# Optimization experiments

Hardware: AMD Instinct MI355X
Metric: run time of the kernel (lower is better)

Reference implementation:

```python
import jax, jax.numpy as jnp
import numpy as np
from jax.scipy.special import logsumexp


def setup_inputs() -> dict:
    key = jax.random.key(0)
    k = jax.random.split(key, 8)
    B, T, K, L = 32, 128, 16, 16
    s = 0.05
    y_batch = jax.random.uniform(k[0], (B, T, 1, 28, 28), dtype=jnp.float32)
    enc_w1 = jax.random.normal(k[1], (400, 784), dtype=jnp.float32) * s
    enc_b1 = jnp.zeros((400,), jnp.float32)
    enc_w2 = jax.random.normal(k[2], (2 * L, 400), dtype=jnp.float32) * s
    enc_b2 = jnp.zeros((2 * L,), jnp.float32)
    dec_fc_w = jax.random.normal(k[3], (400, L + K), dtype=jnp.float32) * s
    dec_fc_b = jnp.zeros((400,), jnp.float32)
    dec_w = jax.random.normal(k[4], (784, 400), dtype=jnp.float32) * s
    dec_b = jnp.zeros((784,), jnp.float32)
    log_pi = jnp.zeros((K,), jnp.float32)
    log_A = jax.random.normal(k[5], (K, K), dtype=jnp.float32)
    log_A = log_A.at[jnp.arange(K), jnp.arange(K)].set(-1e9)  # fill_diagonal_(-1e9)
    eps = jax.random.normal(k[6], (B * T, L), dtype=jnp.float32)
    return dict(y_batch=y_batch, enc_w1=enc_w1, enc_b1=enc_b1, enc_w2=enc_w2,
                enc_b2=enc_b2, dec_fc_w=dec_fc_w, dec_fc_b=dec_fc_b, dec_w=dec_w,
                dec_b=dec_b, log_pi=log_pi, log_A=log_A, eps=eps)


def reference(y_batch, enc_w1, enc_b1, enc_w2, enc_b2, dec_fc_w, dec_fc_b,
              dec_w, dec_b, log_pi, log_A, eps):
    B, T = y_batch.shape[0], y_batch.shape[1]
    K = log_pi.shape[0]
    L = eps.shape[1]
    N = B * T
    # ---- VAE emission log-likelihoods (compute_log_bk); dropout in eval mode ----
    y_flat = y_batch.reshape(N, 784)
    h = jax.nn.relu(y_flat @ enc_w1.T + enc_b1)                 # [N,400]
    ml = h @ enc_w2.T + enc_b2                                   # [N,2L]
    mu, logvar = ml[:, :L], ml[:, L:]
    z = mu + eps * jnp.exp(0.5 * logvar)                         # reparameterize
    # decode(z, one_hot(k)) for all k at once: split cat-linear into z part + k column
    Wz, Wx = dec_fc_w[:, :L], dec_fc_w[:, L:]                    # [400,L],[400,K]
    base = z @ Wz.T + dec_fc_b                                   # [N,400]
    hk = jax.nn.relu(base[None, :, :] + Wx.T[:, None, :])        # [K,N,400]
    y_rec = jax.nn.sigmoid(jnp.einsum('knh,oh->kno', hk, dec_w) + dec_b)  # [K,N,784]
    # binary_cross_entropy with torch's log clamp at -100
    logp = jnp.clip(jnp.log(y_rec), -100.0, None)
    log1mp = jnp.clip(jnp.log(1.0 - y_rec), -100.0, None)
    bce = -(y_flat[None] * logp + (1.0 - y_flat[None]) * log1mp)  # [K,N,784]
    recon = bce.sum(-1) / 100.0                                   # [K,N]
    log_bk = (-recon).reshape(K, B, T).transpose(1, 2, 0)         # [B,T,K]
    # ---- forward-backward in log domain ----
    lp = jnp.log(jax.nn.softmax(log_pi) + 1e-9)
    lA = jnp.log(jax.nn.softmax(log_A, axis=1) + 1e-9)
    lb_rest = jnp.moveaxis(log_bk[:, 1:], 1, 0)                   # [T-1,B,K]
    a0 = lp + log_bk[:, 0]                                        # [B,K]

    def fstep(prev, lb_t):
        cur = logsumexp(prev[:, :, None] + lA[None], axis=1) + lb_t
        return cur, cur

    _, alphas = jax.lax.scan(fstep, a0, lb_rest)
    log_alpha = jnp.concatenate([a0[:, None], jnp.moveaxis(alphas, 0, 1)], axis=1)  # [B,T,K]

    bT = jnp.zeros((B, K), log_bk.dtype)

    def bstep(nxt, lb_t1):
        cur = logsumexp(lA[None] + (lb_t1 + nxt)[:, None, :], axis=2)
        return cur, cur

    _, betas = jax.lax.scan(bstep, bT, lb_rest, reverse=True)     # betas[t] = beta_t, t=0..T-2
    log_beta = jnp.concatenate([jnp.moveaxis(betas, 0, 1), bT[:, None]], axis=1)  # [B,T,K]

    lg = log_alpha + log_beta
    log_gamma = lg - logsumexp(lg, axis=2, keepdims=True)

    lxi = (log_alpha[:, :-1, :, None] + lA[None, None]
           + (log_bk[:, 1:] + log_beta[:, 1:])[:, :, None, :])    # [B,T-1,K,K]
    lxi = lxi - logsumexp(lxi, axis=(2, 3), keepdims=True)
    return jnp.exp(log_gamma), jnp.exp(lxi)
```

## Files before the change

kernel.cpp:

```cpp
#include <hip/hip_runtime.h>
#include <math.h>


typedef _Float16 h8v __attribute__((ext_vector_type(8)));
typedef _Float16 h4v __attribute__((ext_vector_type(4)));
typedef float f16v __attribute__((ext_vector_type(16)));

__global__ __launch_bounds__(256)
void k_prep(const float* __restrict__ dw, const float* __restrict__ ew1,
            _Float16* __restrict__ dwh, _Float16* __restrict__ w1h) {
  int idx = blockIdx.x * 256 + threadIdx.x;
  if (idx < 896 * 448) {
    int o = idx / 448, h2 = idx - o * 448;
    float v = (o < 784 && h2 < 400) ? dw[o * 400 + h2] : 0.f;
    dwh[idx] = (_Float16)v;
  } else if (idx < 896 * 448 + 512 * 800) {
    int j = idx - 896 * 448;
    int i = j / 800, kc = j - i * 800;
    float v = (i < 400 && kc < 784) ? ew1[i * 784 + kc] : 0.f;
    w1h[j] = (_Float16)v;
  }
}

#define E1ST 40
__global__ __launch_bounds__(256, 2)
void k_enc1(const float* __restrict__ y, const _Float16* __restrict__ w1h,
            const float* __restrict__ b1, float* __restrict__ hout) {
  __shared__ __align__(16) _Float16 Ah[64 * E1ST];
  __shared__ __align__(16) _Float16 Bh[128 * E1ST];
  const int tid = threadIdx.x;
  const int i0 = blockIdx.x * 128;
  const int n0 = blockIdx.y * 64;
  const int wav = tid >> 6, lane = tid & 63;
  const int wn = wav >> 1, wi = wav & 1;
  const int ln = lane & 31, kg = lane >> 5;

  f16v acc[2];
#pragma unroll
  for (int j = 0; j < 2; ++j)
#pragma unroll
    for (int r = 0; r < 16; ++r) acc[j][r] = 0.f;

  const int ar = tid >> 3, ac4 = (tid & 7) * 4;
  const int br = tid >> 2, bg = (tid & 3) * 8;

#pragma unroll 1
  for (int hc = 0; hc < 25; ++hc) {
    const int h0 = hc * 32;
    __syncthreads();
#pragma unroll
    for (int it = 0; it < 2; ++it) {
      int r = ar + 32 * it;
      float4 a = make_float4(0.f, 0.f, 0.f, 0.f);
      if (h0 + ac4 < 784) a = *(const float4*)&y[(n0 + r) * 784 + h0 + ac4];
      h4v hv;
      hv[0] = (_Float16)a.x; hv[1] = (_Float16)a.y;
      hv[2] = (_Float16)a.z; hv[3] = (_Float16)a.w;
      *(h4v*)&Ah[r * E1ST + ac4] = hv;
    }
#pragma unroll
    for (int it = 0; it < 2; ++it) {
      int r = br + 64 * it;
      *(h8v*)&Bh[r * E1ST + bg] = *(const h8v*)&w1h[(i0 + r) * 800 + h0 + bg];
    }
    __syncthreads();
#pragma unroll
    for (int kk = 0; kk < 2; ++kk) {
      const int ko = kk * 16 + kg * 8;
      h8v a  = *(const h8v*)&Ah[(wn * 32 + ln) * E1ST + ko];
      h8v b0 = *(const h8v*)&Bh[(wi * 64 + ln) * E1ST + ko];
      h8v b1 = *(const h8v*)&Bh[(wi * 64 + 32 + ln) * E1ST + ko];
      acc[0] = __builtin_amdgcn_mfma_f32_32x32x16_f16(a, b0, acc[0], 0, 0, 0);
      acc[1] = __builtin_amdgcn_mfma_f32_32x32x16_f16(a, b1, acc[1], 0, 0, 0);
    }
  }
#pragma unroll
  for (int j = 0; j < 2; ++j) {
    const int i = i0 + wi * 64 + j * 32 + ln;
    if (i < 400) {
      const float bias = b1[i];
#pragma unroll
      for (int reg = 0; reg < 16; ++reg) {
        const int row = n0 + wn * 32 + (reg & 3) + 8 * (reg >> 2) + 4 * kg;
        hout[row * 400 + i] = fmaxf(acc[j][reg] + bias, 0.f);
      }
    }
  }
}

__global__ __launch_bounds__(128, 4)
void k_enc2z(const float* __restrict__ h, const float* __restrict__ w2,
             const float* __restrict__ b2, const float* __restrict__ eps,
             float* __restrict__ z) {
  __shared__ __align__(16) float h_lds[4 * 400];
  __shared__ __align__(16) float w2_lds[32 * 404];
  __shared__ float ml_lds[4 * 32];
  const int tid = threadIdx.x;
  const int n0 = blockIdx.x * 4;
  for (int idx = tid; idx < 400; idx += 128) {
    int r = idx / 100, c = idx % 100;
    *(float4*)&h_lds[r * 400 + c * 4] = *(const float4*)&h[(n0 + r) * 400 + c * 4];
  }
  for (int idx = tid; idx < 3200; idx += 128) {
    int r = idx / 100, c = idx % 100;
    *(float4*)&w2_lds[r * 404 + c * 4] = *(const float4*)&w2[r * 400 + c * 4];
  }
  __syncthreads();
  const int c_ = tid & 31, n_ = tid >> 5;
  float acc = 0.f;
  for (int q = 0; q < 100; ++q) {
    float4 hv = *(const float4*)&h_lds[n_ * 400 + q * 4];
    float4 wv = *(const float4*)&w2_lds[c_ * 404 + q * 4];
    acc += hv.x * wv.x + hv.y * wv.y + hv.z * wv.z + hv.w * wv.w;
  }
  ml_lds[n_ * 32 + c_] = acc + b2[c_];
  __syncthreads();
  if (tid < 64) {
    int n2 = tid >> 4, l = tid & 15;
    float mu = ml_lds[n2 * 32 + l];
    float lv = ml_lds[n2 * 32 + 16 + l];
    z[(n0 + n2) * 16 + l] = mu + eps[(n0 + n2) * 16 + l] * expf(0.5f * lv);
  }
}

__global__ __launch_bounds__(256, 4)
void k_base(const float* __restrict__ z, const float* __restrict__ dfw,
            const float* __restrict__ dfb, float* __restrict__ basep) {
  __shared__ float z_lds[16 * 16];
  __shared__ __align__(16) float wz_lds[400 * 20];
  const int tid = threadIdx.x;
  const int n0 = blockIdx.x * 16;
  if (tid < 64) {
    int n = tid >> 2, c = (tid & 3) * 4;
    *(float4*)&z_lds[n * 16 + c] = *(const float4*)&z[(n0 + n) * 16 + c];
  }
  for (int idx = tid; idx < 1600; idx += 256) {
    int i = idx >> 2, c = (idx & 3) * 4;
    *(float4*)&wz_lds[i * 20 + c] = *(const float4*)&dfw[i * 32 + c];
  }
  __syncthreads();
  for (int idx = tid; idx < 7168; idx += 256) {
    int n = idx / 448, i = idx - n * 448;
    float acc = 0.f;
    if (i < 400) {
      acc = dfb[i];
#pragma unroll
      for (int q = 0; q < 4; ++q) {
        float4 zv = *(const float4*)&z_lds[n * 16 + q * 4];
        float4 wv = *(const float4*)&wz_lds[i * 20 + q * 4];
        acc += zv.x * wv.x + zv.y * wv.y + zv.z * wv.z + zv.w * wv.w;
      }
    }
    basep[(n0 + n) * 448 + i] = acc;
  }
}

#define DST 72
__global__ __launch_bounds__(256, 2)
void k_dec(const float* __restrict__ basep, const float* __restrict__ dfw,
           const _Float16* __restrict__ dwh, const float* __restrict__ decb,
           const float* __restrict__ y, float* __restrict__ lb) {
  __shared__ __align__(16) _Float16 Ah[128 * DST];
  __shared__ __align__(16) _Float16 Bh[128 * DST];
  __shared__ float wx[448];
  __shared__ float red[256];

  const int tid = threadIdx.x;
  const int k = blockIdx.x;
  const int n0 = blockIdx.y * 128;
  const int wav = tid >> 6, lane = tid & 63;
  const int wn = wav >> 1, wo = wav & 1;
  const int ln = lane & 31, kg = lane >> 5;

  for (int i = tid; i < 448; i += 256) wx[i] = (i < 400) ? dfw[i * 32 + 16 + k] : 0.f;

  float pr[2][16];
#pragma unroll
  for (int i = 0; i < 2; ++i)
#pragma unroll
    for (int r = 0; r < 16; ++r) pr[i][r] = 0.f;

  const int ar = tid >> 4, ac4 = (tid & 15) * 4;
  const int br = tid >> 3, bg = (tid & 7) * 8;
  const float* aptr = basep + (long)(n0 + ar) * 448 + ac4;

  float4 apf[8];
#pragma unroll
  for (int it = 0; it < 8; ++it) apf[it] = *(const float4*)&aptr[(16 * it) * 448];

#pragma unroll 1
  for (int ot = 0; ot < 7; ++ot) {
    const int o0 = ot * 128;
    const bool full = (ot < 6);
    f16v acc[2][2];
#pragma unroll
    for (int i = 0; i < 2; ++i)
#pragma unroll
      for (int j = 0; j < 2; ++j)
#pragma unroll
        for (int r = 0; r < 16; ++r) acc[i][j][r] = 0.f;

#pragma unroll 1
    for (int hc = 0; hc < 7; ++hc) {
      const int h0 = hc * 64;
      h8v bpf[4];
#pragma unroll
      for (int it = 0; it < 4; ++it)
        bpf[it] = *(const h8v*)&dwh[(o0 + br + 32 * it) * 448 + h0 + bg];
      __syncthreads();
      {
        float4 w = *(const float4*)&wx[h0 + ac4];
#pragma unroll
        for (int it = 0; it < 8; ++it) {
          int r = ar + 16 * it;
          h4v hv;
          hv[0] = (_Float16)fmaxf(apf[it].x + w.x, 0.f);
          hv[1] = (_Float16)fmaxf(apf[it].y + w.y, 0.f);
          hv[2] = (_Float16)fmaxf(apf[it].z + w.z, 0.f);
          hv[3] = (_Float16)fmaxf(apf[it].w + w.w, 0.f);
          *(h4v*)&Ah[r * DST + ac4] = hv;
        }
      }
#pragma unroll
      for (int it = 0; it < 4; ++it)
        *(h8v*)&Bh[(br + 32 * it) * DST + bg] = bpf[it];
      __syncthreads();
      if (!(ot == 6 && hc == 6)) {
        const int hn = (hc == 6) ? 0 : (hc + 1) * 64;
#pragma unroll
        for (int it = 0; it < 8; ++it)
          apf[it] = *(const float4*)&aptr[(16 * it) * 448 + hn];
      }
#pragma unroll
      for (int kk = 0; kk < 4; ++kk) {
        const int ko = kk * 16 + kg * 8;
        h8v a0 = *(const h8v*)&Ah[(wn * 64 + ln) * DST + ko];
        h8v a1 = *(const h8v*)&Ah[(wn * 64 + 32 + ln) * DST + ko];
        h8v b0 = *(const h8v*)&Bh[(wo * 64 + ln) * DST + ko];
        h8v b1 = *(const h8v*)&Bh[(wo * 64 + 32 + ln) * DST + ko];
        if (full) {
          acc[0][0] = __builtin_amdgcn_mfma_f32_32x32x16_f16(a0, b0, acc[0][0], 0, 0, 0);
          acc[1][0] = __builtin_amdgcn_mfma_f32_32x32x16_f16(a1, b0, acc[1][0], 0, 0, 0);
          acc[0][1] = __builtin_amdgcn_mfma_f32_32x32x16_f16(a0, b1, acc[0][1], 0, 0, 0);
          acc[1][1] = __builtin_amdgcn_mfma_f32_32x32x16_f16(a1, b1, acc[1][1], 0, 0, 0);
        } else if (wo == 0) {
          acc[0][0] = __builtin_amdgcn_mfma_f32_32x32x16_f16(a0, b0, acc[0][0], 0, 0, 0);
          acc[1][0] = __builtin_amdgcn_mfma_f32_32x32x16_f16(a1, b0, acc[1][0], 0, 0, 0);
        }
      }
    }
#pragma unroll
    for (int j = 0; j < 2; ++j) {
      const int o = o0 + wo * 64 + j * 32 + ln;
      const bool valid = (o < 784);
      const float bias = valid ? decb[o] : 0.f;
#pragma unroll
      for (int i = 0; i < 2; ++i) {
        if (valid) {
#pragma unroll
          for (int reg = 0; reg < 16; ++reg) {
            const int row = wn * 64 + i * 32 + (reg & 3) + 8 * (reg >> 2) + 4 * kg;
            float x = acc[i][j][reg] + bias;
            float yv = y[(n0 + row) * 784 + o];
            float spx = fmaxf(x, 0.f) + __logf(1.f + __expf(-fabsf(x)));
            float t2 = fminf(spx, 100.f);
            float t1 = fminf(spx - x, 100.f);
            pr[i][reg] += t2 + yv * (t1 - t2);
          }
        }
      }
    }
  }
#pragma unroll
  for (int i = 0; i < 2; ++i)
#pragma unroll
    for (int reg = 0; reg < 16; ++reg) {
      float v = pr[i][reg];
      v += __shfl_xor(v, 1, 64);
      v += __shfl_xor(v, 2, 64);
      v += __shfl_xor(v, 4, 64);
      v += __shfl_xor(v, 8, 64);
      v += __shfl_xor(v, 16, 64);
      if (ln == 0) {
        const int row = wn * 64 + i * 32 + (reg & 3) + 8 * (reg >> 2) + 4 * kg;
        red[wo * 128 + row] = v;
      }
    }
  __syncthreads();
  if (tid < 128) {
    float s = red[tid] + red[128 + tid];
    lb[(n0 + tid) * 16 + k] = -(s / 100.0f);
  }
}

__global__ __launch_bounds__(256, 2)
void k_hmm(const float* __restrict__ lb, const float* __restrict__ lpi,
           const float* __restrict__ lA, float* __restrict__ out,
           float* __restrict__ g_ah, float* __restrict__ g_pb,
           float* __restrict__ g_sinv, float* __restrict__ g_Al) {
  __shared__ float btl[128 * 16];
  __shared__ float ah[128 * 16];
  __shared__ float bh[128 * 16];
  __shared__ float braw[128 * 16];
  __shared__ float A_l[16 * 17];
  __shared__ float pi_l[16];
  const int tid = threadIdx.x;
  const int b = blockIdx.x;

  for (int idx = tid; idx < 512; idx += 256)
    *(float4*)&btl[idx * 4] = *(const float4*)&lb[b * 2048 + idx * 4];
  if (tid < 16) {
    const int j = tid;
    float m = -1e30f;
#pragma unroll
    for (int q = 0; q < 16; ++q) m = fmaxf(m, lA[j * 16 + q]);
    float e[16]; float s = 0.f;
#pragma unroll
    for (int q = 0; q < 16; ++q) { e[q] = expf(lA[j * 16 + q] - m); s += e[q]; }
    float inv = 1.f / s;
#pragma unroll
    for (int q = 0; q < 16; ++q) {
      float v = e[q] * inv + 1e-9f;
      A_l[j * 17 + q] = v;
      g_Al[j * 16 + q] = v;
    }
  } else if (tid == 16) {
    float m = -1e30f;
#pragma unroll
    for (int q = 0; q < 16; ++q) m = fmaxf(m, lpi[q]);
    float e[16]; float s = 0.f;
#pragma unroll
    for (int q = 0; q < 16; ++q) { e[q] = expf(lpi[q] - m); s += e[q]; }
    float inv = 1.f / s;
#pragma unroll
    for (int q = 0; q < 16; ++q) pi_l[q] = e[q] * inv + 1e-9f;
  }
  __syncthreads();
  if (tid < 128) {
    const int t = tid;
    float v[16]; float m = -1e30f;
#pragma unroll
    for (int q = 0; q < 16; ++q) { v[q] = btl[t * 16 + q]; m = fmaxf(m, v[q]); }
#pragma unroll
    for (int q = 0; q < 16; ++q) btl[t * 16 + q] = expf(v[q] - m);
  }
  __syncthreads();
  const int lane = tid & 63;
  const int kk = lane & 15, grp = lane >> 4;
  if (tid < 64) {
    float v0 = pi_l[kk] * btl[kk];
    float ss0 = v0;
    ss0 += __shfl_xor(ss0, 1, 64); ss0 += __shfl_xor(ss0, 2, 64);
    ss0 += __shfl_xor(ss0, 4, 64); ss0 += __shfl_xor(ss0, 8, 64);
    if (grp == 0) ah[kk] = v0 / ss0;
    for (int t = 1; t < 128; ++t) {
      float acc = 0.f;
#pragma unroll
      for (int jj = 0; jj < 4; ++jj) {
        int j = grp * 4 + jj;
        acc = fmaf(ah[(t - 1) * 16 + j], A_l[j * 17 + kk], acc);
      }
      acc += __shfl_xor(acc, 16, 64);
      acc += __shfl_xor(acc, 32, 64);
      float v = acc * btl[t * 16 + kk];
      float ss = v;
      ss += __shfl_xor(ss, 1, 64); ss += __shfl_xor(ss, 2, 64);
      ss += __shfl_xor(ss, 4, 64); ss += __shfl_xor(ss, 8, 64);
      if (grp == 0) ah[t * 16 + kk] = v / ss;
    }
  } else if (tid < 128) {
    if (grp == 0) bh[127 * 16 + kk] = 1.f;
    for (int t = 126; t >= 0; --t) {
      float acc = 0.f;
#pragma unroll
      for (int q = 0; q < 4; ++q) {
        int k2 = grp * 4 + q;
        acc = fmaf(A_l[kk * 17 + k2], btl[(t + 1) * 16 + k2] * bh[(t + 1) * 16 + k2], acc);
      }
      acc += __shfl_xor(acc, 16, 64);
      acc += __shfl_xor(acc, 32, 64);
      float ss = acc;
      ss += __shfl_xor(ss, 1, 64); ss += __shfl_xor(ss, 2, 64);
      ss += __shfl_xor(ss, 4, 64); ss += __shfl_xor(ss, 8, 64);
      if (grp == 0) { braw[t * 16 + kk] = acc; bh[t * 16 + kk] = acc / ss; }
    }
  }
  __syncthreads();
  if (tid < 128) {
    const int t = tid;
    float g[16]; float s2 = 0.f;
#pragma unroll
    for (int q = 0; q < 16; ++q) { g[q] = ah[t * 16 + q] * bh[t * 16 + q]; s2 += g[q]; }
    float inv = 1.f / s2;
#pragma unroll
    for (int c = 0; c < 4; ++c) {
      float4 o;
      o.x = g[c * 4 + 0] * inv; o.y = g[c * 4 + 1] * inv;
      o.z = g[c * 4 + 2] * inv; o.w = g[c * 4 + 3] * inv;
      *(float4*)&out[(b * 128 + t) * 16 + c * 4] = o;
      float4 av = *(float4*)&ah[t * 16 + c * 4];
      *(float4*)&g_ah[(b * 128 + t) * 16 + c * 4] = av;
      float4 p;
      p.x = btl[t * 16 + c * 4 + 0] * bh[t * 16 + c * 4 + 0];
      p.y = btl[t * 16 + c * 4 + 1] * bh[t * 16 + c * 4 + 1];
      p.z = btl[t * 16 + c * 4 + 2] * bh[t * 16 + c * 4 + 2];
      p.w = btl[t * 16 + c * 4 + 3] * bh[t * 16 + c * 4 + 3];
      *(float4*)&g_pb[(b * 128 + t) * 16 + c * 4] = p;
    }
  } else {
    const int t = tid - 128;
    if (t < 127) {
      float s2 = 0.f;
#pragma unroll
      for (int q = 0; q < 16; ++q) s2 += ah[t * 16 + q] * braw[t * 16 + q];
      g_sinv[b * 128 + t] = 1.f / s2;
    }
  }
}

__global__ __launch_bounds__(256)
void k_xi(const float* __restrict__ g_ah, const float* __restrict__ g_pb,
          const float* __restrict__ g_sinv, const float* __restrict__ g_Al,
          float* __restrict__ out) {
  const int b = blockIdx.x, t = blockIdx.y;
  const int tid = threadIdx.x;
  const int j = tid >> 4, k2 = tid & 15;
  float val = g_ah[(b * 128 + t) * 16 + j] * g_Al[j * 16 + k2] *
              g_pb[(b * 128 + t + 1) * 16 + k2] * g_sinv[b * 128 + t];
  out[65536 + (b * 127 + t) * 256 + tid] = val;
}

extern "C" void kernel_launch(void* const* d_in, const int* in_sizes, int n_in,
                              void* d_out, int out_size, void* d_ws, size_t ws_size,
                              hipStream_t stream) {
  (void)in_sizes; (void)n_in; (void)out_size; (void)ws_size;
  const float* y   = (const float*)d_in[0];
  const float* ew1 = (const float*)d_in[1];
  const float* eb1 = (const float*)d_in[2];
  const float* ew2 = (const float*)d_in[3];
  const float* eb2 = (const float*)d_in[4];
  const float* dfw = (const float*)d_in[5];
  const float* dfb = (const float*)d_in[6];
  const float* dw  = (const float*)d_in[7];
  const float* db  = (const float*)d_in[8];
  const float* lpi = (const float*)d_in[9];
  const float* lA  = (const float*)d_in[10];
  const float* eps = (const float*)d_in[11];
  float* out = (float*)d_out;

  float* ws = (float*)d_ws;
  float* h      = ws;
  float* basep  = ws;
  float* z      = ws + 1835008;
  float* lb     = z + 65536;
  _Float16* dwh = (_Float16*)(lb + 65536);
  _Float16* w1h = dwh + 896 * 448;
  float* g_ah   = (float*)(w1h + 512 * 800);
  float* g_pb   = g_ah + 65536;
  float* g_sinv = g_pb + 65536;
  float* g_Al   = g_sinv + 4096;

  k_prep<<<3168, 256, 0, stream>>>(dw, ew1, dwh, w1h);
  k_enc1<<<dim3(4, 64), 256, 0, stream>>>(y, w1h, eb1, h);
  k_enc2z<<<1024, 128, 0, stream>>>(h, ew2, eb2, eps, z);
  k_base<<<256, 256, 0, stream>>>(z, dfw, dfb, basep);
  k_dec<<<dim3(16, 32), 256, 0, stream>>>(basep, dfw, dwh, db, y, lb);
  k_hmm<<<32, 256, 0, stream>>>(lb, lpi, lA, out, g_ah, g_pb, g_sinv, g_Al);
  k_xi<<<dim3(32, 127), 256, 0, stream>>>(g_ah, g_pb, g_sinv, g_Al, out);
}
```

Before: 338.9 us.

## Fuse encoder stages, split decoder over output tiles, fold xi into HMM kernel

Several changes at once. The w1 fp16 pre-conversion moves into k_enc1, which now converts on the fly and writes h as fp16. enc2, z and base are fused into a single k_ezb kernel that also zeroes lb. k_dec is split so each block handles one output tile, giving 3584 blocks with prefetched B tiles, and partial BCE sums are accumulated into lb with atomicAdd. The HMM forward/backward recursions now keep data in registers and shuffles with rcp instead of division, and the xi output kernel is merged into k_hmm. Together these remove launches and intermediate traffic, at the cost of atomics and a per-block basep reload for every output tile.

```diff
diff --git a/kernel.cpp b/kernel.cpp
--- a/kernel.cpp
+++ b/kernel.cpp
@@ -7,25 +7,19 @@
 typedef float f16v __attribute__((ext_vector_type(16)));
 
 __global__ __launch_bounds__(256)
-void k_prep(const float* __restrict__ dw, const float* __restrict__ ew1,
-            _Float16* __restrict__ dwh, _Float16* __restrict__ w1h) {
+void k_prep(const float* __restrict__ dw, _Float16* __restrict__ dwh) {
   int idx = blockIdx.x * 256 + threadIdx.x;
   if (idx < 896 * 448) {
     int o = idx / 448, h2 = idx - o * 448;
     float v = (o < 784 && h2 < 400) ? dw[o * 400 + h2] : 0.f;
     dwh[idx] = (_Float16)v;
-  } else if (idx < 896 * 448 + 512 * 800) {
-    int j = idx - 896 * 448;
-    int i = j / 800, kc = j - i * 800;
-    float v = (i < 400 && kc < 784) ? ew1[i * 784 + kc] : 0.f;
-    w1h[j] = (_Float16)v;
   }
 }
 
 #define E1ST 40
 __global__ __launch_bounds__(256, 2)
-void k_enc1(const float* __restrict__ y, const _Float16* __restrict__ w1h,
-            const float* __restrict__ b1, float* __restrict__ hout) {
+void k_enc1(const float* __restrict__ y, const float* __restrict__ w1,
+            const float* __restrict__ b1, _Float16* __restrict__ hout) {
   __shared__ __align__(16) _Float16 Ah[64 * E1ST];
   __shared__ __align__(16) _Float16 Bh[128 * E1ST];
   const int tid = threadIdx.x;
@@ -42,7 +36,6 @@
     for (int r = 0; r < 16; ++r) acc[j][r] = 0.f;
 
   const int ar = tid >> 3, ac4 = (tid & 7) * 4;
-  const int br = tid >> 2, bg = (tid & 3) * 8;
 
 #pragma unroll 1
   for (int hc = 0; hc < 25; ++hc) {
@@ -59,9 +52,16 @@
       *(h4v*)&Ah[r * E1ST + ac4] = hv;
     }
 #pragma unroll
-    for (int it = 0; it < 2; ++it) {
-      int r = br + 64 * it;
-      *(h8v*)&Bh[r * E1ST + bg] = *(const h8v*)&w1h[(i0 + r) * 800 + h0 + bg];
+    for (int it = 0; it < 4; ++it) {
+      int idx = tid + it * 256;
+      int r = idx >> 3, c4 = (idx & 7) * 4;
+      int gi = i0 + r, gh = h0 + c4;
+      float4 v = make_float4(0.f, 0.f, 0.f, 0.f);
+      if (gi < 400 && gh + 3 < 784) v = *(const float4*)&w1[gi * 784 + gh];
+      h4v hv;
+      hv[0] = (_Float16)v.x; hv[1] = (_Float16)v.y;
+      hv[2] = (_Float16)v.z; hv[3] = (_Float16)v.w;
+      *(h4v*)&Bh[r * E1ST + c4] = hv;
     }
     __syncthreads();
 #pragma unroll
@@ -69,9 +69,9 @@
       const int ko = kk * 16 + kg * 8;
       h8v a  = *(const h8v*)&Ah[(wn * 32 + ln) * E1ST + ko];
       h8v b0 = *(const h8v*)&Bh[(wi * 64 + ln) * E1ST + ko];
-      h8v b1 = *(const h8v*)&Bh[(wi * 64 + 32 + ln) * E1ST + ko];
+      h8v b1v = *(const h8v*)&Bh[(wi * 64 + 32 + ln) * E1ST + ko];
       acc[0] = __builtin_amdgcn_mfma_f32_32x32x16_f16(a, b0, acc[0], 0, 0, 0);
-      acc[1] = __builtin_amdgcn_mfma_f32_32x32x16_f16(a, b1, acc[1], 0, 0, 0);
+      acc[1] = __builtin_amdgcn_mfma_f32_32x32x16_f16(a, b1v, acc[1], 0, 0, 0);
     }
   }
 #pragma unroll
@@ -82,61 +82,47 @@
 #pragma unroll
       for (int reg = 0; reg < 16; ++reg) {
         const int row = n0 + wn * 32 + (reg & 3) + 8 * (reg >> 2) + 4 * kg;
-        hout[row * 400 + i] = fmaxf(acc[j][reg] + bias, 0.f);
-      }
-    }
-  }
-}
-
-__global__ __launch_bounds__(128, 4)
-void k_enc2z(const float* __restrict__ h, const float* __restrict__ w2,
-             const float* __restrict__ b2, const float* __restrict__ eps,
-             float* __restrict__ z) {
-  __shared__ __align__(16) float h_lds[4 * 400];
-  __shared__ __align__(16) float w2_lds[32 * 404];
-  __shared__ float ml_lds[4 * 32];
-  const int tid = threadIdx.x;
-  const int n0 = blockIdx.x * 4;
-  for (int idx = tid; idx < 400; idx += 128) {
-    int r = idx / 100, c = idx % 100;
-    *(float4*)&h_lds[r * 400 + c * 4] = *(const float4*)&h[(n0 + r) * 400 + c * 4];
-  }
-  for (int idx = tid; idx < 3200; idx += 128) {
-    int r = idx / 100, c = idx % 100;
-    *(float4*)&w2_lds[r * 404 + c * 4] = *(const float4*)&w2[r * 400 + c * 4];
-  }
-  __syncthreads();
-  const int c_ = tid & 31, n_ = tid >> 5;
-  float acc = 0.f;
-  for (int q = 0; q < 100; ++q) {
-    float4 hv = *(const float4*)&h_lds[n_ * 400 + q * 4];
-    float4 wv = *(const float4*)&w2_lds[c_ * 404 + q * 4];
-    acc += hv.x * wv.x + hv.y * wv.y + hv.z * wv.z + hv.w * wv.w;
-  }
-  ml_lds[n_ * 32 + c_] = acc + b2[c_];
-  __syncthreads();
-  if (tid < 64) {
-    int n2 = tid >> 4, l = tid & 15;
-    float mu = ml_lds[n2 * 32 + l];
-    float lv = ml_lds[n2 * 32 + 16 + l];
-    z[(n0 + n2) * 16 + l] = mu + eps[(n0 + n2) * 16 + l] * expf(0.5f * lv);
-  }
-}
-
-__global__ __launch_bounds__(256, 4)
-void k_base(const float* __restrict__ z, const float* __restrict__ dfw,
-            const float* __restrict__ dfb, float* __restrict__ basep) {
-  __shared__ float z_lds[16 * 16];
-  __shared__ __align__(16) float wz_lds[400 * 20];
+        hout[row * 400 + i] = (_Float16)fmaxf(acc[j][reg] + bias, 0.f);
+      }
+    }
+  }
+}
+
+__global__ __launch_bounds__(256, 2)
+void k_ezb(const _Float16* __restrict__ h, const float* __restrict__ w2,
+           const float* __restrict__ b2, const float* __restrict__ eps,
+           const float* __restrict__ dfw, const float* __restrict__ dfb,
+           float* __restrict__ basep, float* __restrict__ lb) {
+  __shared__ __align__(16) float h_lds[16 * 400];
+  __shared__ float ml[16 * 32];
+  __shared__ float zs[16 * 16];
   const int tid = threadIdx.x;
   const int n0 = blockIdx.x * 16;
-  if (tid < 64) {
-    int n = tid >> 2, c = (tid & 3) * 4;
-    *(float4*)&z_lds[n * 16 + c] = *(const float4*)&z[(n0 + n) * 16 + c];
-  }
-  for (int idx = tid; idx < 1600; idx += 256) {
-    int i = idx >> 2, c = (idx & 3) * 4;
-    *(float4*)&wz_lds[i * 20 + c] = *(const float4*)&dfw[i * 32 + c];
+  for (int idx = tid; idx < 800; idx += 256) {
+    int r = idx / 50, c8 = (idx % 50) * 8;
+    h8v v = *(const h8v*)&h[(n0 + r) * 400 + c8];
+#pragma unroll
+    for (int e = 0; e < 8; ++e) h_lds[r * 400 + c8 + e] = (float)v[e];
+  }
+  lb[n0 * 16 + tid] = 0.f;
+  __syncthreads();
+#pragma unroll
+  for (int it = 0; it < 2; ++it) {
+    int task = tid + it * 256;
+    int c = task & 31, n = task >> 5;
+    float acc = 0.f;
+    for (int q = 0; q < 100; ++q) {
+      float4 hv = *(const float4*)&h_lds[n * 400 + q * 4];
+      float4 wv = *(const float4*)&w2[c * 400 + q * 4];
+      acc += hv.x * wv.x + hv.y * wv.y + hv.z * wv.z + hv.w * wv.w;
+    }
+    ml[n * 32 + c] = acc + b2[c];
+  }
+  __syncthreads();
+  {
+    int n = tid >> 4, l = tid & 15;
+    float mu = ml[n * 32 + l], lv = ml[n * 32 + 16 + l];
+    zs[n * 16 + l] = mu + eps[(n0 + n) * 16 + l] * expf(0.5f * lv);
   }
   __syncthreads();
   for (int idx = tid; idx < 7168; idx += 256) {
@@ -146,8 +132,8 @@
       acc = dfb[i];
 #pragma unroll
       for (int q = 0; q < 4; ++q) {
-        float4 zv = *(const float4*)&z_lds[n * 16 + q * 4];
-        float4 wv = *(const float4*)&wz_lds[i * 20 + q * 4];
+        float4 zv = *(const float4*)&zs[n * 16 + q * 4];
+        float4 wv = *(const float4*)&dfw[i * 32 + q * 4];
         acc += zv.x * wv.x + zv.y * wv.y + zv.z * wv.z + zv.w * wv.w;
       }
     }
@@ -166,144 +152,137 @@
   __shared__ float red[256];
 
   const int tid = threadIdx.x;
-  const int k = blockIdx.x;
-  const int n0 = blockIdx.y * 128;
+  const int w = blockIdx.x;
+  const int ot = w >> 9;
+  const int r0 = w & 511;
+  const int k  = (r0 >> 3) & 15;
+  const int nt = (r0 & 7) + 8 * (r0 >> 7);
+  const int n0 = nt * 128;
+  const int o0 = ot * 128;
+  const bool full = (ot < 6);
+
   const int wav = tid >> 6, lane = tid & 63;
   const int wn = wav >> 1, wo = wav & 1;
   const int ln = lane & 31, kg = lane >> 5;
 
   for (int i = tid; i < 448; i += 256) wx[i] = (i < 400) ? dfw[i * 32 + 16 + k] : 0.f;
 
-  float pr[2][16];
-#pragma unroll
-  for (int i = 0; i < 2; ++i)
-#pragma unroll
-    for (int r = 0; r < 16; ++r) pr[i][r] = 0.f;
-
   const int ar = tid >> 4, ac4 = (tid & 15) * 4;
   const int br = tid >> 3, bg = (tid & 7) * 8;
   const float* aptr = basep + (long)(n0 + ar) * 448 + ac4;
 
   float4 apf[8];
+  h8v bpf[4];
 #pragma unroll
   for (int it = 0; it < 8; ++it) apf[it] = *(const float4*)&aptr[(16 * it) * 448];
+#pragma unroll
+  for (int it = 0; it < 4; ++it)
+    bpf[it] = *(const h8v*)&dwh[(o0 + br + 32 * it) * 448 + bg];
+
+  f16v acc[2][2];
+#pragma unroll
+  for (int i = 0; i < 2; ++i)
+#pragma unroll
+    for (int j = 0; j < 2; ++j)
+#pragma unroll
+      for (int r = 0; r < 16; ++r) acc[i][j][r] = 0.f;
 
 #pragma unroll 1
-  for (int ot = 0; ot < 7; ++ot) {
-    const int o0 = ot * 128;
-    const bool full = (ot < 6);
-    f16v acc[2][2];
-#pragma unroll
-    for (int i = 0; i < 2; ++i)
-#pragma unroll
-      for (int j = 0; j < 2; ++j)
-#pragma unroll
-        for (int r = 0; r < 16; ++r) acc[i][j][r] = 0.f;
-
-#pragma unroll 1
-    for (int hc = 0; hc < 7; ++hc) {
-      const int h0 = hc * 64;
-      h8v bpf[4];
+  for (int hc = 0; hc < 7; ++hc) {
+    const int h0 = hc * 64;
+    __syncthreads();
+    {
+      float4 wv = *(const float4*)&wx[h0 + ac4];
+#pragma unroll
+      for (int it = 0; it < 8; ++it) {
+        int rr = ar + 16 * it;
+        h4v hv;
+        hv[0] = (_Float16)fmaxf(apf[it].x + wv.x, 0.f);
+        hv[1] = (_Float16)fmaxf(apf[it].y + wv.y, 0.f);
+        hv[2] = (_Float16)fmaxf(apf[it].z + wv.z, 0.f);
+        hv[3] = (_Float16)fmaxf(apf[it].w + wv.w, 0.f);
+        *(h4v*)&Ah[rr * DST + ac4] = hv;
+      }
+    }
+#pragma unroll
+    for (int it = 0; it < 4; ++it)
+      *(h8v*)&Bh[(br + 32 * it) * DST + bg] = bpf[it];
+    __syncthreads();
+    if (hc < 6) {
+      const int hn = (hc + 1) * 64;
+#pragma unroll
+      for (int it = 0; it < 8; ++it)
+        apf[it] = *(const float4*)&aptr[(16 * it) * 448 + hn];
 #pragma unroll
       for (int it = 0; it < 4; ++it)
-        bpf[it] = *(const h8v*)&dwh[(o0 + br + 32 * it) * 448 + h0 + bg];
-      __syncthreads();
-      {
-        float4 w = *(const float4*)&wx[h0 + ac4];
-#pragma unroll
-        for (int it = 0; it < 8; ++it) {
-          int r = ar + 16 * it;
-          h4v hv;
-          hv[0] = (_Float16)fmaxf(apf[it].x + w.x, 0.f);
-          hv[1] = (_Float16)fmaxf(apf[it].y + w.y, 0.f);
-          hv[2] = (_Float16)fmaxf(apf[it].z + w.z, 0.f);
-          hv[3] = (_Float16)fmaxf(apf[it].w + w.w, 0.f);
-          *(h4v*)&Ah[r * DST + ac4] = hv;
-        }
-      }
-#pragma unroll
-      for (int it = 0; it < 4; ++it)
-        *(h8v*)&Bh[(br + 32 * it) * DST + bg] = bpf[it];
-      __syncthreads();
-      if (!(ot == 6 && hc == 6)) {
-        const int hn = (hc == 6) ? 0 : (hc + 1) * 64;
-#pragma unroll
-        for (int it = 0; it < 8; ++it)
-          apf[it] = *(const float4*)&aptr[(16 * it) * 448 + hn];
-      }
-#pragma unroll
-      for (int kk = 0; kk < 4; ++kk) {
-        const int ko = kk * 16 + kg * 8;
-        h8v a0 = *(const h8v*)&Ah[(wn * 64 + ln) * DST + ko];
-        h8v a1 = *(const h8v*)&Ah[(wn * 64 + 32 + ln) * DST + ko];
-        h8v b0 = *(const h8v*)&Bh[(wo * 64 + ln) * DST + ko];
-        h8v b1 = *(const h8v*)&Bh[(wo * 64 + 32 + ln) * DST + ko];
-        if (full) {
-          acc[0][0] = __builtin_amdgcn_mfma_f32_32x32x16_f16(a0, b0, acc[0][0], 0, 0, 0);
-          acc[1][0] = __builtin_amdgcn_mfma_f32_32x32x16_f16(a1, b0, acc[1][0], 0, 0, 0);
-          acc[0][1] = __builtin_amdgcn_mfma_f32_32x32x16_f16(a0, b1, acc[0][1], 0, 0, 0);
-          acc[1][1] = __builtin_amdgcn_mfma_f32_32x32x16_f16(a1, b1, acc[1][1], 0, 0, 0);
-        } else if (wo == 0) {
-          acc[0][0] = __builtin_amdgcn_mfma_f32_32x32x16_f16(a0, b0, acc[0][0], 0, 0, 0);
-          acc[1][0] = __builtin_amdgcn_mfma_f32_32x32x16_f16(a1, b0, acc[1][0], 0, 0, 0);
-        }
-      }
-    }
-#pragma unroll
-    for (int j = 0; j < 2; ++j) {
-      const int o = o0 + wo * 64 + j * 32 + ln;
-      const bool valid = (o < 784);
-      const float bias = valid ? decb[o] : 0.f;
-#pragma unroll
-      for (int i = 0; i < 2; ++i) {
-        if (valid) {
-#pragma unroll
-          for (int reg = 0; reg < 16; ++reg) {
-            const int row = wn * 64 + i * 32 + (reg & 3) + 8 * (reg >> 2) + 4 * kg;
-            float x = acc[i][j][reg] + bias;
-            float yv = y[(n0 + row) * 784 + o];
-            float spx = fmaxf(x, 0.f) + __logf(1.f + __expf(-fabsf(x)));
-            float t2 = fminf(spx, 100.f);
-            float t1 = fminf(spx - x, 100.f);
-            pr[i][reg] += t2 + yv * (t1 - t2);
-          }
-        }
-      }
-    }
-  }
+        bpf[it] = *(const h8v*)&dwh[(o0 + br + 32 * it) * 448 + hn + bg];
+    }
+#pragma unroll
+    for (int kk = 0; kk < 4; ++kk) {
+      const int ko = kk * 16 + kg * 8;
+      h8v a0 = *(const h8v*)&Ah[(wn * 64 + ln) * DST + ko];
+      h8v a1 = *(const h8v*)&Ah[(wn * 64 + 32 + ln) * DST + ko];
+      h8v b0 = *(const h8v*)&Bh[(wo * 64 + ln) * DST + ko];
+      h8v b1v = *(const h8v*)&Bh[(wo * 64 + 32 + ln) * DST + ko];
+      if (full) {
+        acc[0][0] = __builtin_amdgcn_mfma_f32_32x32x16_f16(a0, b0, acc[0][0], 0, 0, 0);
+        acc[1][0] = __builtin_amdgcn_mfma_f32_32x32x16_f16(a1, b0, acc[1][0], 0, 0, 0);
+        acc[0][1] = __builtin_amdgcn_mfma_f32_32x32x16_f16(a0, b1v, acc[0][1], 0, 0, 0);
+        acc[1][1] = __builtin_amdgcn_mfma_f32_32x32x16_f16(a1, b1v, acc[1][1], 0, 0, 0);
+      } else if (wo == 0) {
+        acc[0][0] = __builtin_amdgcn_mfma_f32_32x32x16_f16(a0, b0, acc[0][0], 0, 0, 0);
+        acc[1][0] = __builtin_amdgcn_mfma_f32_32x32x16_f16(a1, b0, acc[1][0], 0, 0, 0);
+      }
+    }
+  }
+  const int oa = o0 + wo * 64 + ln;
+  const int ob = oa + 32;
+  const float biasa = (oa < 784) ? decb[oa] : 0.f;
+  const float biasb = (ob < 784) ? decb[ob] : 0.f;
 #pragma unroll
   for (int i = 0; i < 2; ++i)
 #pragma unroll
     for (int reg = 0; reg < 16; ++reg) {
-      float v = pr[i][reg];
+      const int row = wn * 64 + i * 32 + (reg & 3) + 8 * (reg >> 2) + 4 * kg;
+      float v = 0.f;
+      if (oa < 784) {
+        float x = acc[i][0][reg] + biasa;
+        float yv = y[(n0 + row) * 784 + oa];
+        float spx = fmaxf(x, 0.f) + __logf(1.f + __expf(-fabsf(x)));
+        float t2 = fminf(spx, 100.f);
+        float t1 = fminf(spx - x, 100.f);
+        v += t2 + yv * (t1 - t2);
+      }
+      if (ob < 784) {
+        float x = acc[i][1][reg] + biasb;
+        float yv = y[(n0 + row) * 784 + ob];
+        float spx = fmaxf(x, 0.f) + __logf(1.f + __expf(-fabsf(x)));
+        float t2 = fminf(spx, 100.f);
+        float t1 = fminf(spx - x, 100.f);
+        v += t2 + yv * (t1 - t2);
+      }
       v += __shfl_xor(v, 1, 64);
       v += __shfl_xor(v, 2, 64);
       v += __shfl_xor(v, 4, 64);
       v += __shfl_xor(v, 8, 64);
       v += __shfl_xor(v, 16, 64);
-      if (ln == 0) {
-        const int row = wn * 64 + i * 32 + (reg & 3) + 8 * (reg >> 2) + 4 * kg;
-        red[wo * 128 + row] = v;
-      }
-    }
-  __syncthreads();
-  if (tid < 128) {
-    float s = red[tid] + red[128 + tid];
-    lb[(n0 + tid) * 16 + k] = -(s / 100.0f);
-  }
+      if (ln == 0) red[wo * 128 + row] = v;
+    }
+  __syncthreads();
+  if (tid < 128)
+    atomicAdd(&lb[(n0 + tid) * 16 + k], -(red[tid] + red[128 + tid]) * 0.01f);
 }
 
 __global__ __launch_bounds__(256, 2)
 void k_hmm(const float* __restrict__ lb, const float* __restrict__ lpi,
-           const float* __restrict__ lA, float* __restrict__ out,
-           float* __restrict__ g_ah, float* __restrict__ g_pb,
-           float* __restrict__ g_sinv, float* __restrict__ g_Al) {
+           const float* __restrict__ lA, float* __restrict__ out) {
   __shared__ float btl[128 * 16];
   __shared__ float ah[128 * 16];
   __shared__ float bh[128 * 16];
   __shared__ float braw[128 * 16];
   __shared__ float A_l[16 * 17];
   __shared__ float pi_l[16];
+  __shared__ float sinv_s[128];
   const int tid = threadIdx.x;
   const int b = blockIdx.x;
 
@@ -319,11 +298,7 @@
     for (int q = 0; q < 16; ++q) { e[q] = expf(lA[j * 16 + q] - m); s += e[q]; }
     float inv = 1.f / s;
 #pragma unroll
-    for (int q = 0; q < 16; ++q) {
-      float v = e[q] * inv + 1e-9f;
-      A_l[j * 17 + q] = v;
-      g_Al[j * 16 + q] = v;
-    }
+    for (int q = 0; q < 16; ++q) A_l[j * 17 + q] = e[q] * inv + 1e-9f;
   } else if (tid == 16) {
     float m = -1e30f;
 #pragma unroll
@@ -348,41 +323,56 @@
   const int lane = tid & 63;
   const int kk = lane & 15, grp = lane >> 4;
   if (tid < 64) {
-    float v0 = pi_l[kk] * btl[kk];
-    float ss0 = v0;
-    ss0 += __shfl_xor(ss0, 1, 64); ss0 += __shfl_xor(ss0, 2, 64);
-    ss0 += __shfl_xor(ss0, 4, 64); ss0 += __shfl_xor(ss0, 8, 64);
-    if (grp == 0) ah[kk] = v0 / ss0;
+    float Ar[4];
+#pragma unroll
+    for (int jj = 0; jj < 4; ++jj) Ar[jj] = A_l[(grp * 4 + jj) * 17 + kk];
+    float v = pi_l[kk] * btl[kk];
+    float ss = v;
+    ss += __shfl_xor(ss, 1, 64); ss += __shfl_xor(ss, 2, 64);
+    ss += __shfl_xor(ss, 4, 64); ss += __shfl_xor(ss, 8, 64);
+    float a = v * __builtin_amdgcn_rcpf(ss);
+    if (grp == 0) ah[kk] = a;
+    float btc = btl[16 + kk];
+#pragma unroll 1
     for (int t = 1; t < 128; ++t) {
       float acc = 0.f;
 #pragma unroll
-      for (int jj = 0; jj < 4; ++jj) {
-        int j = grp * 4 + jj;
-        acc = fmaf(ah[(t - 1) * 16 + j], A_l[j * 17 + kk], acc);
-      }
+      for (int jj = 0; jj < 4; ++jj)
+        acc = fmaf(Ar[jj], __shfl(a, grp * 4 + jj, 64), acc);
       acc += __shfl_xor(acc, 16, 64);
       acc += __shfl_xor(acc, 32, 64);
-      float v = acc * btl[t * 16 + kk];
-      float ss = v;
-      ss += __shfl_xor(ss, 1, 64); ss += __shfl_xor(ss, 2, 64);
-      ss += __shfl_xor(ss, 4, 64); ss += __shfl_xor(ss, 8, 64);
-      if (grp == 0) ah[t * 16 + kk] = v / ss;
+      float btn = (t < 127) ? btl[(t + 1) * 16 + kk] : 0.f;
+      float v2 = acc * btc;
+      float s2 = v2;
+      s2 += __shfl_xor(s2, 1, 64); s2 += __shfl_xor(s2, 2, 64);
+      s2 += __shfl_xor(s2, 4, 64); s2 += __shfl_xor(s2, 8, 64);
+      a = v2 * __builtin_amdgcn_rcpf(s2);
+      if (grp == 0) ah[t * 16 + kk] = a;
+      btc = btn;
     }
   } else if (tid < 128) {
+    float Ar[4];
+#pragma unroll
+    for (int q = 0; q < 4; ++q) Ar[q] = A_l[kk * 17 + grp * 4 + q];
     if (grp == 0) bh[127 * 16 + kk] = 1.f;
+    float p = btl[127 * 16 + kk];
+    float btc = btl[126 * 16 + kk];
+#pragma unroll 1
     for (int t = 126; t >= 0; --t) {
       float acc = 0.f;
 #pragma unroll
-      for (int q = 0; q < 4; ++q) {
-        int k2 = grp * 4 + q;
-        acc = fmaf(A_l[kk * 17 + k2], btl[(t + 1) * 16 + k2] * bh[(t + 1) * 16 + k2], acc);
-      }
+      for (int q = 0; q < 4; ++q)
+        acc = fmaf(Ar[q], __shfl(p, grp * 4 + q, 64), acc);
       acc += __shfl_xor(acc, 16, 64);
       acc += __shfl_xor(acc, 32, 64);
+      float btn = (t > 0) ? btl[(t - 1) * 16 + kk] : 0.f;
       float ss = acc;
       ss += __shfl_xor(ss, 1, 64); ss += __shfl_xor(ss, 2, 64);
       ss += __shfl_xor(ss, 4, 64); ss += __shfl_xor(ss, 8, 64);
-      if (grp == 0) { braw[t * 16 + kk] = acc; bh[t * 16 + kk] = acc / ss; }
+      float bnorm = acc * __builtin_amdgcn_rcpf(ss);
+      if (grp == 0) { braw[t * 16 + kk] = acc; bh[t * 16 + kk] = bnorm; }
+      p = btc * bnorm;
+      btc = btn;
     }
   }
   __syncthreads();
@@ -398,14 +388,6 @@
       o.x = g[c * 4 + 0] * inv; o.y = g[c * 4 + 1] * inv;
       o.z = g[c * 4 + 2] * inv; o.w = g[c * 4 + 3] * inv;
       *(float4*)&out[(b * 128 + t) * 16 + c * 4] = o;
-      float4 av = *(float4*)&ah[t * 16 + c * 4];
-      *(float4*)&g_ah[(b * 128 + t) * 16 + c * 4] = av;
-      float4 p;
-      p.x = btl[t * 16 + c * 4 + 0] * bh[t * 16 + c * 4 + 0];
-      p.y = btl[t * 16 + c * 4 + 1] * bh[t * 16 + c * 4 + 1];
-      p.z = btl[t * 16 + c * 4 + 2] * bh[t * 16 + c * 4 + 2];
-      p.w = btl[t * 16 + c * 4 + 3] * bh[t * 16 + c * 4 + 3];
-      *(float4*)&g_pb[(b * 128 + t) * 16 + c * 4] = p;
     }
   } else {
     const int t = tid - 128;
@@ -413,21 +395,21 @@
       float s2 = 0.f;
 #pragma unroll
       for (int q = 0; q < 16; ++q) s2 += ah[t * 16 + q] * braw[t * 16 + q];
-      g_sinv[b * 128 + t] = 1.f / s2;
-    }
-  }
-}
-
-__global__ __launch_bounds__(256)
-void k_xi(const float* __restrict__ g_ah, const float* __restrict__ g_pb,
-          const float* __restrict__ g_sinv, const float* __restrict__ g_Al,
-          float* __restrict__ out) {
-  const int b = blockIdx.x, t = blockIdx.y;
-  const int tid = threadIdx.x;
-  const int j = tid >> 4, k2 = tid & 15;
-  float val = g_ah[(b * 128 + t) * 16 + j] * g_Al[j * 16 + k2] *
-              g_pb[(b * 128 + t + 1) * 16 + k2] * g_sinv[b * 128 + t];
-  out[65536 + (b * 127 + t) * 256 + tid] = val;
+      sinv_s[t] = 1.f / s2;
+    }
+  }
+  __syncthreads();
+  {
+    const int j = tid >> 4, k2 = tid & 15;
+    const float Ajk = A_l[j * 17 + k2];
+    float* xo = out + 65536 + b * 127 * 256;
+#pragma unroll 1
+    for (int t = 0; t < 127; ++t) {
+      float val = ah[t * 16 + j] * Ajk *
+                  (btl[(t + 1) * 16 + k2] * bh[(t + 1) * 16 + k2]) * sinv_s[t];
+      xo[t * 256 + tid] = val;
+    }
+  }
 }
 
 extern "C" void kernel_launch(void* const* d_in, const int* in_sizes, int n_in,
@@ -449,22 +431,14 @@
   float* out = (float*)d_out;
 
   float* ws = (float*)d_ws;
-  float* h      = ws;
   float* basep  = ws;
-  float* z      = ws + 1835008;
-  float* lb     = z + 65536;
+  _Float16* h16 = (_Float16*)(ws + 1835008);
+  float* lb     = ws + 1835008 + 819200;
   _Float16* dwh = (_Float16*)(lb + 65536);
-  _Float16* w1h = dwh + 896 * 448;
-  float* g_ah   = (float*)(w1h + 512 * 800);
-  float* g_pb   = g_ah + 65536;
-  float* g_sinv = g_pb + 65536;
-  float* g_Al   = g_sinv + 4096;
-
-  k_prep<<<3168, 256, 0, stream>>>(dw, ew1, dwh, w1h);
-  k_enc1<<<dim3(4, 64), 256, 0, stream>>>(y, w1h, eb1, h);
-  k_enc2z<<<1024, 128, 0, stream>>>(h, ew2, eb2, eps, z);
-  k_base<<<256, 256, 0, stream>>>(z, dfw, dfb, basep);
-  k_dec<<<dim3(16, 32), 256, 0, stream>>>(basep, dfw, dwh, db, y, lb);
-  k_hmm<<<32, 256, 0, stream>>>(lb, lpi, lA, out, g_ah, g_pb, g_sinv, g_Al);
-  k_xi<<<dim3(32, 127), 256, 0, stream>>>(g_ah, g_pb, g_sinv, g_Al, out);
-}
+
+  k_prep<<<1568, 256, 0, stream>>>(dw, dwh);
+  k_enc1<<<dim3(4, 64), 256, 0, stream>>>(y, ew1, eb1, h16);
+  k_ezb<<<256, 256, 0, stream>>>(h16, ew2, eb2, eps, dfw, dfb, basep, lb);
+  k_dec<<<3584, 256, 0, stream>>>(basep, dfw, dwh, db, y, lb);
+  k_hmm<<<32, 256, 0, stream>>>(lb, lpi, lA, out);
+}
```

Measured after the change: 433.9 us. 1.28x slower.
